# Kernel tuning notes

Hardware: AMD Instinct MI355X
Metric: run time of the kernel (lower is better)

The kernel has to match this reference:

```python
import jax, jax.numpy as jnp
import numpy as np

L, B, T = 2048, 2048, 7


def setup_inputs() -> dict:
    key = jax.random.key(0)
    k = jax.random.split(key, 6)
    emissions = jax.random.normal(k[0], (L, B, T), dtype=jnp.float32)
    tags = jax.random.randint(k[1], (L, B), 0, T, dtype=jnp.int32)
    qmask = jnp.zeros((L, B), dtype=jnp.int32)   # single speaker per conversation
    mask = jnp.ones((L, B), dtype=jnp.int32)     # first timestep must be all-on
    u = lambda kk, shp: jax.random.uniform(kk, shp, jnp.float32, -0.1, 0.1)
    return {
        'emissions': emissions, 'tags': tags, 'qmask': qmask, 'mask': mask,
        'start_transitions': u(k[2], (T,)),
        'end_transitions': u(k[3], (T,)),
        'self_transitions': u(k[4], (T, T)),
        'other_transitions': u(k[5], (T, T)),
    }


def _crf_llh(emissions, tags, qmask, mask, start_transitions, end_transitions,
             self_transitions, other_transitions):
    # emissions: [L, B, T]; tags/qmask/mask: [L, B]
    Lx, Bx, Tx = emissions.shape
    maskf = mask.astype(emissions.dtype)
    # contagion[i]: utterance i follows an utterance by a different speaker
    contagion = qmask[1:] != qmask[:-1]                                  # [L-1, B]
    brange = jnp.arange(Bx)

    # ---- numerator: score of the gold tag path (CRF._compute_score) ----
    em_tag = jnp.take_along_axis(emissions, tags[:, :, None], axis=2)[:, :, 0]   # [L, B]
    trans_tag = jnp.where(contagion,
                          other_transitions[tags[:-1], tags[1:]],
                          self_transitions[tags[:-1], tags[1:]])                 # [L-1, B]
    score = start_transitions[tags[0]] + em_tag[0]
    score = score + jnp.sum((trans_tag + em_tag[1:]) * maskf[1:], axis=0)
    seq_ends = mask.sum(axis=0) - 1                                              # [B]
    score = score + end_transitions[tags[seq_ends, brange]]

    # ---- denominator: partition function via sequential log-sum-exp scan ----
    def step(alpha, xs):
        em_i, cont_i, m_i = xs
        trans = jnp.where(cont_i[:, None, None],
                          other_transitions[None], self_transitions[None])       # [B, T, T]
        new = jax.nn.logsumexp(alpha[:, :, None] + trans, axis=1) + em_i         # [B, T]
        alpha = jnp.where(m_i[:, None] > 0, new, alpha)
        return alpha, None

    alpha0 = start_transitions[None, :] + emissions[0]                           # [B, T]
    alpha, _ = jax.lax.scan(step, alpha0, (emissions[1:], contagion, mask[1:]))
    logZ = jax.nn.logsumexp(alpha + end_transitions[None, :], axis=1)            # [B]

    return jnp.sum(score - logZ)   # reduction='sum'


def reference(emissions, tags, qmask, mask, start_transitions, end_transitions,
              self_transitions, other_transitions):
    return _crf_llh(emissions, tags, qmask, mask, start_transitions,
                    end_transitions, self_transitions, other_transitions)
```

## Files before the change

kernel.cpp:

```cpp
#include <hip/hip_runtime.h>
#include <hip/hip_bf16.h>

#define LSEQ 2048
#define BB   2048
#define TT   7
#define NFLD 17

typedef float f4 __attribute__((ext_vector_type(4)));

__device__ __forceinline__ void ld7(const float* __restrict__ p, float* e) {
  f4 lo, hi;
  __builtin_memcpy(&lo, p, 16);
  __builtin_memcpy(&hi, p + 3, 16);
  e[0] = lo.x; e[1] = lo.y; e[2] = lo.z; e[3] = lo.w;
  e[4] = hi.y; e[5] = hi.z; e[6] = hi.w;
}

template<int KCH>
__global__ __launch_bounds__(256)
void crf_chunk_kernel(const float* __restrict__ em,
                      const int*   __restrict__ tags,
                      const int*   __restrict__ qmask,
                      const int*   __restrict__ mask,
                      const float* __restrict__ self_t,
                      const float* __restrict__ other_t,
                      float* __restrict__ recs) {
  constexpr int CC   = LSEQ / KCH;
  constexpr int NG   = KCH * BB;
  constexpr int NB   = (CC < 4) ? CC : 4;
  constexpr int NFWD = NG / 256;
  __shared__ float sE[2][49];
  __shared__ float sT[2][49];
  int tid = threadIdx.x;
  if (tid < 49) {
    float sv = self_t[tid], ov = other_t[tid];
    sE[0][tid] = __expf(sv); sE[1][tid] = __expf(ov);
    sT[0][tid] = sv;         sT[1][tid] = ov;
  }
  __syncthreads();

  float Es[49];
  int loadedCont = -1;
  auto loadEs = [&](int cf) {
#pragma unroll
    for (int k = 0; k < 49; ++k)
      Es[k] = __int_as_float(
          __builtin_amdgcn_readfirstlane(__float_as_int(sE[cf][k])));
    loadedCont = cf;
  };

  int bid = blockIdx.x;
  if (bid < NFWD) {
    int g = bid * 256 + tid;
    int b = g & (BB - 1);
    int c = g >> 11;
    float v[7] = {1.f,1.f,1.f,1.f,1.f,1.f,1.f};
    float sc = 0.f, Lv = 0.f;
    int mc = 0, tp, qp;
    int i0 = c * CC;
    if (c == 0) { mc = mask[b]; tp = tags[b]; qp = qmask[b]; }
    else { size_t pb = (size_t)(i0 - 1) * BB + b; tp = tags[pb]; qp = qmask[pb]; }

    auto LDF = [&](int s, float* e, int& tg, int& qm, int& mi) {
      size_t base = (size_t)(i0 + s) * BB + b;
      ld7(em + base * TT, e);
      tg = tags[base]; qm = qmask[base]; mi = mask[base];
    };

    float e0[7], e1[7];
    int tg0, qm0, mi0, tg1, qm1, mi1;
    LDF(0, e0, tg0, qm0, mi0);

    for (int j = 0; j < CC; ++j) {
      bool more = (j + 1 < CC);
      if (more) LDF(j + 1, e1, tg1, qm1, mi1);

      int mi = (c == 0 && j == 0) ? 0 : mi0;
      int cont = (qm0 != qp) ? 1 : 0;
      int cf = __builtin_amdgcn_readfirstlane(cont);
      bool uni = __all(cont == cf);
      float ee[7];
#pragma unroll
      for (int t = 0; t < 7; ++t) ee[t] = __expf(e0[t]);
      float etag = e0[0];
#pragma unroll
      for (int t = 1; t < 7; ++t) etag = (tg0 == t) ? e0[t] : etag;
      float ttag = sT[cont][tp * 7 + tg0];
      if (mi) { sc += ttag + etag; ++mc; }
      tp = tg0; qp = qm0;

      float a[7] = {0.f,0.f,0.f,0.f,0.f,0.f,0.f};
      if (uni) {
        if (cf != loadedCont) loadEs(cf);
#pragma unroll
        for (int r = 0; r < 7; ++r) {
          float vr = v[r];
#pragma unroll
          for (int t = 0; t < 7; ++t) a[t] = fmaf(vr, Es[r*7+t], a[t]);
        }
      } else {
        loadedCont = -1;
#pragma unroll
        for (int r = 0; r < 7; ++r) {
          float vr = v[r];
#pragma unroll
          for (int t = 0; t < 7; ++t) a[t] = fmaf(vr, sE[cont][r*7+t], a[t]);
        }
      }
#pragma unroll
      for (int t = 0; t < 7; ++t) v[t] = mi ? a[t] * ee[t] : v[t];

      if ((j & 7) == 7) {
        float ss = v[0]+v[1]+v[2]+v[3]+v[4]+v[5]+v[6];
        Lv += logf(ss);
        float inv = 1.0f / ss;
#pragma unroll
        for (int t = 0; t < 7; ++t) v[t] *= inv;
      }
      if (more) {
#pragma unroll
        for (int t = 0; t < 7; ++t) e0[t] = e1[t];
        tg0 = tg1; qm0 = qm1; mi0 = mi1;
      }
    }
    float ss = v[0]+v[1]+v[2]+v[3]+v[4]+v[5]+v[6];
    float inv = 1.0f / ss;
#pragma unroll
    for (int t = 0; t < 7; ++t) recs[(size_t)t * NG + g] = v[t] * inv;
    recs[(size_t)14 * NG + g] = sc;
    recs[(size_t)15 * NG + g] = (float)mc;
    recs[(size_t)16 * NG + g] = Lv + logf(ss);
  } else {
    int g = (bid - NFWD) * 256 + tid;
    int b = g & (BB - 1);
    int c = g >> 11;
    float r[7] = {1.f,1.f,1.f,1.f,1.f,1.f,1.f};
    int ilo = (c == 0) ? 1 : c * CC;

    auto LDB = [&](int s, float* e, int& q, int& q1, int& mi2) {
      size_t base = (size_t)(ilo + NB - 1 - s) * BB + b;
      ld7(em + base * TT, e);
      q = qmask[base]; q1 = qmask[base - BB]; mi2 = mask[base];
    };

    float e0[7], e1[7];
    int q0, q10, m0, q1v, q11, m1;
    LDB(0, e0, q0, q10, m0);

    for (int j = 0; j < NB; ++j) {
      bool more = (j + 1 < NB);
      if (more) LDB(j + 1, e1, q1v, q11, m1);

      int cont = (q0 != q10) ? 1 : 0;
      int cf = __builtin_amdgcn_readfirstlane(cont);
      bool uni = __all(cont == cf);
      float ee[7];
#pragma unroll
      for (int t = 0; t < 7; ++t) ee[t] = __expf(e0[t]);
      float tmp[7];
#pragma unroll
      for (int t = 0; t < 7; ++t) tmp[t] = ee[t] * r[t];
      float a[7] = {0.f,0.f,0.f,0.f,0.f,0.f,0.f};
      if (uni) {
        if (cf != loadedCont) loadEs(cf);
#pragma unroll
        for (int t = 0; t < 7; ++t) {
          float tt = tmp[t];
#pragma unroll
          for (int s2 = 0; s2 < 7; ++s2) a[s2] = fmaf(tt, Es[s2*7+t], a[s2]);
        }
      } else {
        loadedCont = -1;
#pragma unroll
        for (int t = 0; t < 7; ++t) {
          float tt = tmp[t];
#pragma unroll
          for (int s2 = 0; s2 < 7; ++s2) a[s2] = fmaf(tt, sE[cont][s2*7+t], a[s2]);
        }
      }
#pragma unroll
      for (int s2 = 0; s2 < 7; ++s2) r[s2] = m0 ? a[s2] : r[s2];

      if (more) {
#pragma unroll
        for (int t = 0; t < 7; ++t) e0[t] = e1[t];
        q0 = q1v; q10 = q11; m0 = m1;
      }
    }
    float ss = r[0]+r[1]+r[2]+r[3]+r[4]+r[5]+r[6];
    float inv = 1.0f / ss;
#pragma unroll
    for (int t = 0; t < 7; ++t) recs[(size_t)(7 + t) * NG + g] = r[t] * inv;
  }
}

template<int KCH>
__global__ __launch_bounds__(256)
void crf_junction_kernel(const float* __restrict__ recs,
                         const float* __restrict__ em,
                         const int*   __restrict__ tags,
                         const float* __restrict__ start_t,
                         const float* __restrict__ end_t,
                         float* __restrict__ partials) {
  constexpr int NG = KCH * BB;
  int tid = threadIdx.x;
  int g = blockIdx.x * 256 + tid;
  int b = g & (BB - 1);
  int c = g >> 11;
  float rn[7];
#pragma unroll
  for (int t = 0; t < 7; ++t) rn[t] = recs[(size_t)(7 + t) * NG + g];
  float term = recs[(size_t)14 * NG + g] - recs[(size_t)16 * NG + g];
  float dot = 0.f;
  if (c == 0) {
    float e0[7], st[7];
#pragma unroll
    for (int t = 0; t < 7; ++t) { e0[t] = em[(size_t)b * TT + t]; st[t] = start_t[t]; }
#pragma unroll
    for (int t = 0; t < 7; ++t) dot = fmaf(__expf(st[t] + e0[t]), rn[t], dot);
    int tg0 = tags[b];
    float em0t = e0[0], stt = st[0];
#pragma unroll
    for (int t = 1; t < 7; ++t) {
      em0t = (tg0 == t) ? e0[t] : em0t;
      stt  = (tg0 == t) ? st[t] : stt;
    }
    term += stt + em0t;
  } else {
#pragma unroll
    for (int t = 0; t < 7; ++t)
      dot = fmaf(recs[(size_t)t * NG + (g - BB)], rn[t], dot);
  }
  term -= logf(dot);
  if (c == KCH - 1) {
    float fz = 0.f;
#pragma unroll
    for (int t = 0; t < 7; ++t)
      fz = fmaf(recs[(size_t)t * NG + g], __expf(end_t[t]), fz);
    term -= logf(fz);
    float mcf = 0.f;
    for (int cc = 0; cc < KCH; ++cc)
      mcf += recs[(size_t)15 * NG + (size_t)cc * BB + b];
    int se = (int)mcf - 1;
    int te = tags[(size_t)se * BB + b];
    term += end_t[te];
  }
  __shared__ float red[256];
  red[tid] = term;
  __syncthreads();
  for (int off = 128; off > 0; off >>= 1) {
    if (tid < off) red[tid] += red[tid + off];
    __syncthreads();
  }
  if (tid == 0) partials[blockIdx.x] = red[0];
}

__global__ __launch_bounds__(1024)
void crf_reduce_kernel(const float* __restrict__ partials, int n,
                       float* __restrict__ out) {
  __shared__ float s[1024];
  int t = threadIdx.x;
  float v = 0.f;
  for (int i = t; i < n; i += 1024) v += partials[i];
  s[t] = v;
  __syncthreads();
  for (int off = 512; off > 0; off >>= 1) {
    if (t < off) s[t] += s[t + off];
    __syncthreads();
  }
  if (t == 0) out[0] = s[0];
}

extern "C" void kernel_launch(void* const* d_in, const int* in_sizes, int n_in,
                              void* d_out, int out_size, void* d_ws, size_t ws_size,
                              hipStream_t stream) {
  const float* em      = (const float*)d_in[0];
  const int*   tags    = (const int*)d_in[1];
  const int*   qmask   = (const int*)d_in[2];
  const int*   mask    = (const int*)d_in[3];
  const float* start_t = (const float*)d_in[4];
  const float* end_t   = (const float*)d_in[5];
  const float* self_t  = (const float*)d_in[6];
  const float* other_t = (const float*)d_in[7];

  float* recs = (float*)d_ws;

  auto need = [](int kch) {
    size_t ng = (size_t)kch * BB;
    return (NFLD * ng + ng / 256) * sizeof(float);
  };

  if (ws_size >= need(128)) {
    constexpr int KCH = 128;
    constexpr int NG  = KCH * BB;
    float* partials = recs + (size_t)NFLD * NG;
    int fwd_blocks = NG / 256;
    int bwd_blocks = NG / 256;
    crf_chunk_kernel<KCH><<<fwd_blocks + bwd_blocks, 256, 0, stream>>>(
        em, tags, qmask, mask, self_t, other_t, recs);
    crf_junction_kernel<KCH><<<NG / 256, 256, 0, stream>>>(
        recs, em, tags, start_t, end_t, partials);
    crf_reduce_kernel<<<1, 1024, 0, stream>>>(partials, NG / 256, (float*)d_out);
  } else {
    constexpr int KCH = 64;
    constexpr int NG  = KCH * BB;
    float* partials = recs + (size_t)NFLD * NG;
    int fwd_blocks = NG / 256;
    int bwd_blocks = NG / 256;
    crf_chunk_kernel<KCH><<<fwd_blocks + bwd_blocks, 256, 0, stream>>>(
        em, tags, qmask, mask, self_t, other_t, recs);
    crf_junction_kernel<KCH><<<NG / 256, 256, 0, stream>>>(
        recs, em, tags, start_t, end_t, partials);
    crf_reduce_kernel<<<1, 1024, 0, stream>>>(partials, NG / 256, (float*)d_out);
  }
}
```

Baseline: 50.89 us.

## Fuse backward boundary pass into forward chunk thread, reusing buffered emissions

Previously separate blocks ran a short backward pass over the first NB steps of each chunk, reloading emissions, qmask and mask from global memory. Now the forward thread keeps the first NB steps' emissions, contagion flags and masks in registers and runs the backward pass itself after the forward scan. This halves the number of blocks launched and removes the redundant global loads. In exchange each thread carries more registers and a longer serial tail, which could lower occupancy and reduce the parallelism the extra backward blocks used to supply.

```diff
diff --git a/kernel.cpp b/kernel.cpp
--- a/kernel.cpp
+++ b/kernel.cpp
@@ -25,10 +25,9 @@
                       const float* __restrict__ self_t,
                       const float* __restrict__ other_t,
                       float* __restrict__ recs) {
-  constexpr int CC   = LSEQ / KCH;
-  constexpr int NG   = KCH * BB;
-  constexpr int NB   = (CC < 4) ? CC : 4;
-  constexpr int NFWD = NG / 256;
+  constexpr int CC = LSEQ / KCH;
+  constexpr int NG = KCH * BB;
+  constexpr int NB = (CC < 4) ? CC : 4;
   __shared__ float sE[2][49];
   __shared__ float sT[2][49];
   int tid = threadIdx.x;
@@ -49,149 +48,144 @@
     loadedCont = cf;
   };
 
-  int bid = blockIdx.x;
-  if (bid < NFWD) {
-    int g = bid * 256 + tid;
-    int b = g & (BB - 1);
-    int c = g >> 11;
-    float v[7] = {1.f,1.f,1.f,1.f,1.f,1.f,1.f};
-    float sc = 0.f, Lv = 0.f;
-    int mc = 0, tp, qp;
-    int i0 = c * CC;
-    if (c == 0) { mc = mask[b]; tp = tags[b]; qp = qmask[b]; }
-    else { size_t pb = (size_t)(i0 - 1) * BB + b; tp = tags[pb]; qp = qmask[pb]; }
-
-    auto LDF = [&](int s, float* e, int& tg, int& qm, int& mi) {
-      size_t base = (size_t)(i0 + s) * BB + b;
-      ld7(em + base * TT, e);
-      tg = tags[base]; qm = qmask[base]; mi = mask[base];
-    };
-
-    float e0[7], e1[7];
-    int tg0, qm0, mi0, tg1, qm1, mi1;
-    LDF(0, e0, tg0, qm0, mi0);
-
-    for (int j = 0; j < CC; ++j) {
-      bool more = (j + 1 < CC);
-      if (more) LDF(j + 1, e1, tg1, qm1, mi1);
-
-      int mi = (c == 0 && j == 0) ? 0 : mi0;
-      int cont = (qm0 != qp) ? 1 : 0;
-      int cf = __builtin_amdgcn_readfirstlane(cont);
-      bool uni = __all(cont == cf);
-      float ee[7];
-#pragma unroll
-      for (int t = 0; t < 7; ++t) ee[t] = __expf(e0[t]);
-      float etag = e0[0];
-#pragma unroll
-      for (int t = 1; t < 7; ++t) etag = (tg0 == t) ? e0[t] : etag;
-      float ttag = sT[cont][tp * 7 + tg0];
-      if (mi) { sc += ttag + etag; ++mc; }
-      tp = tg0; qp = qm0;
-
-      float a[7] = {0.f,0.f,0.f,0.f,0.f,0.f,0.f};
-      if (uni) {
-        if (cf != loadedCont) loadEs(cf);
-#pragma unroll
-        for (int r = 0; r < 7; ++r) {
-          float vr = v[r];
-#pragma unroll
-          for (int t = 0; t < 7; ++t) a[t] = fmaf(vr, Es[r*7+t], a[t]);
-        }
-      } else {
-        loadedCont = -1;
-#pragma unroll
-        for (int r = 0; r < 7; ++r) {
-          float vr = v[r];
-#pragma unroll
-          for (int t = 0; t < 7; ++t) a[t] = fmaf(vr, sE[cont][r*7+t], a[t]);
-        }
+  int g = blockIdx.x * 256 + tid;
+  int b = g & (BB - 1);
+  int c = g >> 11;
+  float v[7] = {1.f,1.f,1.f,1.f,1.f,1.f,1.f};
+  float sc = 0.f, Lv = 0.f;
+  int mc = 0, tp, qp;
+  int i0 = c * CC;
+  if (c == 0) { mc = mask[b]; tp = tags[b]; qp = qmask[b]; }
+  else { size_t pb = (size_t)(i0 - 1) * BB + b; tp = tags[pb]; qp = qmask[pb]; }
+
+  auto LDF = [&](int s, float* e, int& tg, int& qm, int& mi) {
+    size_t base = (size_t)(i0 + s) * BB + b;
+    ld7(em + base * TT, e);
+    tg = tags[base]; qm = qmask[base]; mi = mask[base];
+  };
+
+  float ub[NB][7];
+  int ucont[NB], umask[NB];
+
+  float e0[7], e1[7];
+  int tg0, qm0, mi0, tg1, qm1, mi1;
+  LDF(0, e0, tg0, qm0, mi0);
+
+  auto FSTEP = [&](const float* e, int tg, int qm, int mi, int& contOut) {
+    int cont = (qm != qp) ? 1 : 0;
+    contOut = cont;
+    int cf = __builtin_amdgcn_readfirstlane(cont);
+    bool uni = __all(cont == cf);
+    float ee[7];
+#pragma unroll
+    for (int t = 0; t < 7; ++t) ee[t] = __expf(e[t]);
+    float etag = e[0];
+#pragma unroll
+    for (int t = 1; t < 7; ++t) etag = (tg == t) ? e[t] : etag;
+    float ttag = sT[cont][tp * 7 + tg];
+    if (mi) { sc += ttag + etag; ++mc; }
+    tp = tg; qp = qm;
+    float a[7] = {0.f,0.f,0.f,0.f,0.f,0.f,0.f};
+    if (uni) {
+      if (cf != loadedCont) loadEs(cf);
+#pragma unroll
+      for (int r = 0; r < 7; ++r) {
+        float vr = v[r];
+#pragma unroll
+        for (int t = 0; t < 7; ++t) a[t] = fmaf(vr, Es[r*7+t], a[t]);
       }
-#pragma unroll
-      for (int t = 0; t < 7; ++t) v[t] = mi ? a[t] * ee[t] : v[t];
-
-      if ((j & 7) == 7) {
-        float ss = v[0]+v[1]+v[2]+v[3]+v[4]+v[5]+v[6];
-        Lv += logf(ss);
-        float inv = 1.0f / ss;
-#pragma unroll
-        for (int t = 0; t < 7; ++t) v[t] *= inv;
+    } else {
+      loadedCont = -1;
+#pragma unroll
+      for (int r = 0; r < 7; ++r) {
+        float vr = v[r];
+#pragma unroll
+        for (int t = 0; t < 7; ++t) a[t] = fmaf(vr, sE[cont][r*7+t], a[t]);
       }
-      if (more) {
-#pragma unroll
-        for (int t = 0; t < 7; ++t) e0[t] = e1[t];
-        tg0 = tg1; qm0 = qm1; mi0 = mi1;
+    }
+#pragma unroll
+    for (int t = 0; t < 7; ++t) v[t] = mi ? a[t] * ee[t] : v[t];
+  };
+
+#pragma unroll
+  for (int j = 0; j < NB; ++j) {
+    LDF(j + 1, e1, tg1, qm1, mi1);
+    int mi = (c == 0 && j == 0) ? 0 : mi0;
+#pragma unroll
+    for (int t = 0; t < 7; ++t) ub[j][t] = e0[t];
+    umask[j] = mi;
+    int contOut;
+    FSTEP(e0, tg0, qm0, mi, contOut);
+    ucont[j] = contOut;
+#pragma unroll
+    for (int t = 0; t < 7; ++t) e0[t] = e1[t];
+    tg0 = tg1; qm0 = qm1; mi0 = mi1;
+  }
+
+  for (int j = NB; j < CC; ++j) {
+    bool more = (j + 1 < CC);
+    if (more) LDF(j + 1, e1, tg1, qm1, mi1);
+    int contOut;
+    FSTEP(e0, tg0, qm0, mi0, contOut);
+    if ((j & 7) == 7) {
+      float ss = v[0]+v[1]+v[2]+v[3]+v[4]+v[5]+v[6];
+      Lv += logf(ss);
+      float inv = 1.0f / ss;
+#pragma unroll
+      for (int t = 0; t < 7; ++t) v[t] *= inv;
+    }
+    if (more) {
+#pragma unroll
+      for (int t = 0; t < 7; ++t) e0[t] = e1[t];
+      tg0 = tg1; qm0 = qm1; mi0 = mi1;
+    }
+  }
+
+  float ss = v[0]+v[1]+v[2]+v[3]+v[4]+v[5]+v[6];
+  float inv = 1.0f / ss;
+#pragma unroll
+  for (int t = 0; t < 7; ++t) recs[(size_t)t * NG + g] = v[t] * inv;
+  recs[(size_t)14 * NG + g] = sc;
+  recs[(size_t)15 * NG + g] = (float)mc;
+  recs[(size_t)16 * NG + g] = Lv + logf(ss);
+
+  float r[7] = {1.f,1.f,1.f,1.f,1.f,1.f,1.f};
+#pragma unroll
+  for (int jj = NB - 1; jj >= 0; --jj) {
+    int cont = ucont[jj], mi = umask[jj];
+    int cf = __builtin_amdgcn_readfirstlane(cont);
+    bool uni = __all(cont == cf);
+    float ee[7];
+#pragma unroll
+    for (int t = 0; t < 7; ++t) ee[t] = __expf(ub[jj][t]);
+    float tmp[7];
+#pragma unroll
+    for (int t = 0; t < 7; ++t) tmp[t] = ee[t] * r[t];
+    float a[7] = {0.f,0.f,0.f,0.f,0.f,0.f,0.f};
+    if (uni) {
+      if (cf != loadedCont) loadEs(cf);
+#pragma unroll
+      for (int t = 0; t < 7; ++t) {
+        float tt = tmp[t];
+#pragma unroll
+        for (int s2 = 0; s2 < 7; ++s2) a[s2] = fmaf(tt, Es[s2*7+t], a[s2]);
       }
-    }
-    float ss = v[0]+v[1]+v[2]+v[3]+v[4]+v[5]+v[6];
-    float inv = 1.0f / ss;
-#pragma unroll
-    for (int t = 0; t < 7; ++t) recs[(size_t)t * NG + g] = v[t] * inv;
-    recs[(size_t)14 * NG + g] = sc;
-    recs[(size_t)15 * NG + g] = (float)mc;
-    recs[(size_t)16 * NG + g] = Lv + logf(ss);
-  } else {
-    int g = (bid - NFWD) * 256 + tid;
-    int b = g & (BB - 1);
-    int c = g >> 11;
-    float r[7] = {1.f,1.f,1.f,1.f,1.f,1.f,1.f};
-    int ilo = (c == 0) ? 1 : c * CC;
-
-    auto LDB = [&](int s, float* e, int& q, int& q1, int& mi2) {
-      size_t base = (size_t)(ilo + NB - 1 - s) * BB + b;
-      ld7(em + base * TT, e);
-      q = qmask[base]; q1 = qmask[base - BB]; mi2 = mask[base];
-    };
-
-    float e0[7], e1[7];
-    int q0, q10, m0, q1v, q11, m1;
-    LDB(0, e0, q0, q10, m0);
-
-    for (int j = 0; j < NB; ++j) {
-      bool more = (j + 1 < NB);
-      if (more) LDB(j + 1, e1, q1v, q11, m1);
-
-      int cont = (q0 != q10) ? 1 : 0;
-      int cf = __builtin_amdgcn_readfirstlane(cont);
-      bool uni = __all(cont == cf);
-      float ee[7];
-#pragma unroll
-      for (int t = 0; t < 7; ++t) ee[t] = __expf(e0[t]);
-      float tmp[7];
-#pragma unroll
-      for (int t = 0; t < 7; ++t) tmp[t] = ee[t] * r[t];
-      float a[7] = {0.f,0.f,0.f,0.f,0.f,0.f,0.f};
-      if (uni) {
-        if (cf != loadedCont) loadEs(cf);
-#pragma unroll
-        for (int t = 0; t < 7; ++t) {
-          float tt = tmp[t];
-#pragma unroll
-          for (int s2 = 0; s2 < 7; ++s2) a[s2] = fmaf(tt, Es[s2*7+t], a[s2]);
-        }
-      } else {
-        loadedCont = -1;
-#pragma unroll
-        for (int t = 0; t < 7; ++t) {
-          float tt = tmp[t];
-#pragma unroll
-          for (int s2 = 0; s2 < 7; ++s2) a[s2] = fmaf(tt, sE[cont][s2*7+t], a[s2]);
-        }
+    } else {
+      loadedCont = -1;
+#pragma unroll
+      for (int t = 0; t < 7; ++t) {
+        float tt = tmp[t];
+#pragma unroll
+        for (int s2 = 0; s2 < 7; ++s2) a[s2] = fmaf(tt, sE[cont][s2*7+t], a[s2]);
       }
-#pragma unroll
-      for (int s2 = 0; s2 < 7; ++s2) r[s2] = m0 ? a[s2] : r[s2];
-
-      if (more) {
-#pragma unroll
-        for (int t = 0; t < 7; ++t) e0[t] = e1[t];
-        q0 = q1v; q10 = q11; m0 = m1;
-      }
-    }
-    float ss = r[0]+r[1]+r[2]+r[3]+r[4]+r[5]+r[6];
-    float inv = 1.0f / ss;
-#pragma unroll
-    for (int t = 0; t < 7; ++t) recs[(size_t)(7 + t) * NG + g] = r[t] * inv;
-  }
+    }
+#pragma unroll
+    for (int s2 = 0; s2 < 7; ++s2) r[s2] = mi ? a[s2] : r[s2];
+  }
+  float sr = r[0]+r[1]+r[2]+r[3]+r[4]+r[5]+r[6];
+  float invr = 1.0f / sr;
+#pragma unroll
+  for (int t = 0; t < 7; ++t) recs[(size_t)(7 + t) * NG + g] = r[t] * invr;
 }
 
 template<int KCH>
@@ -294,9 +288,7 @@
     constexpr int KCH = 128;
     constexpr int NG  = KCH * BB;
     float* partials = recs + (size_t)NFLD * NG;
-    int fwd_blocks = NG / 256;
-    int bwd_blocks = NG / 256;
-    crf_chunk_kernel<KCH><<<fwd_blocks + bwd_blocks, 256, 0, stream>>>(
+    crf_chunk_kernel<KCH><<<NG / 256, 256, 0, stream>>>(
         em, tags, qmask, mask, self_t, other_t, recs);
     crf_junction_kernel<KCH><<<NG / 256, 256, 0, stream>>>(
         recs, em, tags, start_t, end_t, partials);
@@ -305,9 +297,7 @@
     constexpr int KCH = 64;
     constexpr int NG  = KCH * BB;
     float* partials = recs + (size_t)NFLD * NG;
-    int fwd_blocks = NG / 256;
-    int bwd_blocks = NG / 256;
-    crf_chunk_kernel<KCH><<<fwd_blocks + bwd_blocks, 256, 0, stream>>>(
+    crf_chunk_kernel<KCH><<<NG / 256, 256, 0, stream>>>(
         em, tags, qmask, mask, self_t, other_t, recs);
     crf_junction_kernel<KCH><<<NG / 256, 256, 0, stream>>>(
         recs, em, tags, start_t, end_t, partials);
```

New measurement: 48.30 us. 1.05x faster.
